# Kernel tuning notes

Hardware: AMD Instinct MI355X
Metric: run time of the kernel (lower is better)

## Reference

```python
import jax, jax.numpy as jnp
import numpy as np

N_NODES = 100000
N_EDGES = 400000
F_IN = 128
HEADS = 4
C1 = 64   # conv1 out per head
C2 = 128  # conv2 out per head
G = 2048  # num graphs
FP = 2048
HID = 64
NEG_SLOPE = 0.2


def _gat_conv(x, edge_index, W, a_src, a_dst, b, heads, ch):
    """PyG-style GATConv with self-loops, concat=True."""
    n = x.shape[0]
    loops = jnp.arange(n, dtype=edge_index.dtype)
    src = jnp.concatenate([edge_index[0], loops])
    dst = jnp.concatenate([edge_index[1], loops])
    h = (x @ W).reshape(n, heads, ch)                      # [N,H,C]
    e_src = jnp.sum(h * a_src, axis=-1)                    # [N,H]
    e_dst = jnp.sum(h * a_dst, axis=-1)                    # [N,H]
    logits = jax.nn.leaky_relu(e_src[src] + e_dst[dst], NEG_SLOPE)  # [E,H]
    m = jax.ops.segment_max(logits, dst, num_segments=n)   # per-dst max
    p = jnp.exp(logits - m[dst])
    denom = jax.ops.segment_sum(p, dst, num_segments=n)
    alpha = p / denom[dst]                                 # [E,H]
    out = jax.ops.segment_sum(h[src] * alpha[:, :, None], dst, num_segments=n)
    return out.reshape(n, heads * ch) + b


def setup_inputs() -> dict:
    key = jax.random.key(0)
    ks = jax.random.split(key, 16)
    s = 0.05
    inp = {
        "x": jax.random.normal(ks[0], (N_NODES, F_IN), jnp.float32),
        "edge_index": jax.random.randint(ks[1], (2, N_EDGES), 0, N_NODES, jnp.int32),
        "batch": jnp.sort(jax.random.randint(ks[2], (N_NODES,), 0, G, jnp.int32)),
        "fp": jax.random.normal(ks[3], (G, FP), jnp.float32),
        "W1": jax.random.normal(ks[4], (F_IN, HEADS * C1), jnp.float32) * s,
        "a_src1": jax.random.normal(ks[5], (HEADS, C1), jnp.float32) * s,
        "a_dst1": jax.random.normal(ks[6], (HEADS, C1), jnp.float32) * s,
        "b1": jnp.zeros((HEADS * C1,), jnp.float32),
        "W2": jax.random.normal(ks[7], (HEADS * C1, HEADS * C2), jnp.float32) * s,
        "a_src2": jax.random.normal(ks[8], (HEADS, C2), jnp.float32) * s,
        "a_dst2": jax.random.normal(ks[9], (HEADS, C2), jnp.float32) * s,
        "b2": jnp.zeros((HEADS * C2,), jnp.float32),
        "Wfp": jax.random.normal(ks[10], (FP, HID), jnp.float32) * s,
        "bfp": jnp.zeros((HID,), jnp.float32),
        "Wfc1": jax.random.normal(ks[11], (HEADS * C2 + HID, HID), jnp.float32) * s,
        "bfc1": jnp.zeros((HID,), jnp.float32),
        "Wfc2": jax.random.normal(ks[12], (HID, 1), jnp.float32) * s,
        "bfc2": jnp.zeros((1,), jnp.float32),
    }
    return inp


def reference(x, edge_index, batch, fp, W1, a_src1, a_dst1, b1, W2, a_src2, a_dst2, b2,
              Wfp, bfp, Wfc1, bfc1, Wfc2, bfc2):
    h = _gat_conv(x, edge_index, W1, a_src1, a_dst1, b1, HEADS, C1)
    h = jax.nn.elu(h)
    h = _gat_conv(h, edge_index, W2, a_src2, a_dst2, b2, HEADS, C2)
    h = jax.nn.elu(h)
    # global mean pool over graphs
    sums = jax.ops.segment_sum(h, batch, num_segments=G)
    counts = jax.ops.segment_sum(jnp.ones((h.shape[0], 1), h.dtype), batch, num_segments=G)
    pooled = sums / jnp.maximum(counts, 1.0)               # [G, 512]
    fph = fp @ Wfp + bfp                                   # [G, 64]
    z = jnp.concatenate([pooled, fph], axis=1)             # [G, 576]
    z = jax.nn.relu(z @ Wfc1 + bfc1)
    # dropout is identity in eval mode
    return z @ Wfc2 + bfc2                                 # [G, 1]
```

## Files before the change

### kernel.cpp

```cpp
#include <hip/hip_runtime.h>
#include <math.h>

#define NEG_SLOPE 0.2f

typedef __attribute__((ext_vector_type(8))) short bf16x8;
typedef __attribute__((ext_vector_type(4))) float f32x4;
typedef __attribute__((ext_vector_type(2))) float f32x2;

__device__ __forceinline__ float b2f(short s) {
  return __uint_as_float(((unsigned int)(unsigned short)s) << 16);
}
__device__ __forceinline__ unsigned short f2b_rne(float f) {
  unsigned int u = __float_as_uint(f);
  u = (u + 0x7FFF + ((u >> 16) & 1)) >> 16;
  return (unsigned short)u;
}

__device__ __forceinline__ void fp8x8_to_f32(uint2 raw, float* f) {
  f32x2 a = __builtin_amdgcn_cvt_pk_f32_fp8((int)raw.x, false);
  f32x2 b = __builtin_amdgcn_cvt_pk_f32_fp8((int)raw.x, true);
  f32x2 c = __builtin_amdgcn_cvt_pk_f32_fp8((int)raw.y, false);
  f32x2 d = __builtin_amdgcn_cvt_pk_f32_fp8((int)raw.y, true);
  f[0] = a[0]; f[1] = a[1]; f[2] = b[0]; f[3] = b[1];
  f[4] = c[0]; f[5] = c[1]; f[6] = d[0]; f[7] = d[1];
}

__device__ __forceinline__ void gload16(const unsigned short* g, unsigned short* l) {
  __builtin_amdgcn_global_load_lds(
      (const __attribute__((address_space(1))) unsigned int*)g,
      (__attribute__((address_space(3))) unsigned int*)l, 16, 0, 0);
}

__device__ __forceinline__ void tr_one(const float* __restrict__ W,
                                       unsigned short* __restrict__ WT,
                                       int K, int N, int idx)
{
  if (idx < K * N) {
    int k = idx / N, n = idx - k * N;
    WT[(size_t)n * K + k] = f2b_rne(W[idx]);
  }
}

__global__ __launch_bounds__(256) void prep_all(
    const float* __restrict__ x, unsigned short* __restrict__ xb, size_t nx, int B0,
    const float* __restrict__ fp, unsigned short* __restrict__ fpb, size_t nf, int B1,
    const float* __restrict__ W1, unsigned short* __restrict__ W1T,
    const float* __restrict__ W2, unsigned short* __restrict__ W2T,
    const float* __restrict__ Wfp, unsigned short* __restrict__ WfpT,
    const float* __restrict__ Wfc1, unsigned short* __restrict__ Wfc1T)
{
  int b = blockIdx.x;
  const int t = threadIdx.x;
  if (b < B0) {
    size_t i = (size_t)b * 256 + t;
    if (i < nx) xb[i] = f2b_rne(x[i]);
    return;
  }
  b -= B0;
  if (b < B1) {
    size_t i = (size_t)b * 256 + t;
    if (i < nf) fpb[i] = f2b_rne(fp[i]);
    return;
  }
  b -= B1;
  if (b < 128) { tr_one(W1, W1T, 128, 256, b * 256 + t); return; }
  b -= 128;
  if (b < 512) { tr_one(W2, W2T, 256, 512, b * 256 + t); return; }
  b -= 512;
  if (b < 512) { tr_one(Wfp, WfpT, 2048, 64, b * 256 + t); return; }
  b -= 512;
  tr_one(Wfc1, Wfc1T, 576, 64, b * 256 + t);
}

template<int EMODE>
__global__ __launch_bounds__(256) void gemm_mfma(
    const unsigned short* __restrict__ A, const unsigned short* __restrict__ BT,
    unsigned char* __restrict__ Cout, int M, int N, int K,
    const float* __restrict__ a_src, const float* __restrict__ a_dst,
    float* __restrict__ es, float* __restrict__ ed, int nh)
{
  __shared__ unsigned short As[2][128 * 32];
  __shared__ unsigned short Bs[2][128 * 32];
  const int tid  = threadIdx.x;
  const int wave = tid >> 6;
  const int lane = tid & 63;
  const int ln   = lane & 15;
  const int quad = lane >> 4;
  const int wr0  = (wave >> 1) * 64;
  const int wc0  = (wave & 1) * 64;
  const int bm   = blockIdx.y * 128;
  const int bn   = blockIdx.x * 128;

  const int sr = lane >> 2;
  const int sc = (lane & 3) * 8;
  int arow0 = bm + wave * 32 + sr;
  int arow1 = arow0 + 16;
  if (arow0 >= M) arow0 = M - 1;
  if (arow1 >= M) arow1 = M - 1;
  const unsigned short* ga0 = A + (size_t)arow0 * K + sc;
  const unsigned short* ga1 = A + (size_t)arow1 * K + sc;
  const unsigned short* gb0 = BT + (size_t)(bn + wave * 32 + sr) * K + sc;
  const unsigned short* gb1 = BT + (size_t)(bn + wave * 32 + 16 + sr) * K + sc;

  f32x4 acc[4][4];
  const f32x4 z4 = {0.f, 0.f, 0.f, 0.f};
#pragma unroll
  for (int i = 0; i < 4; ++i)
#pragma unroll
    for (int j = 0; j < 4; ++j) acc[i][j] = z4;

  {
    gload16(ga0, &As[0][wave * 1024]);
    gload16(ga1, &As[0][wave * 1024 + 512]);
    gload16(gb0, &Bs[0][wave * 1024]);
    gload16(gb1, &Bs[0][wave * 1024 + 512]);
  }

  int cur = 0;
  for (int k0 = 0; k0 < K; k0 += 32) {
    __syncthreads();
    if (k0 + 32 < K) {
      const int kn = k0 + 32;
      const int nb = cur ^ 1;
      gload16(ga0 + kn, &As[nb][wave * 1024]);
      gload16(ga1 + kn, &As[nb][wave * 1024 + 512]);
      gload16(gb0 + kn, &Bs[nb][wave * 1024]);
      gload16(gb1 + kn, &Bs[nb][wave * 1024 + 512]);
    }
    bf16x8 af[4], bfv[4];
#pragma unroll
    for (int i = 0; i < 4; ++i)
      af[i] = *(const bf16x8*)(&As[cur][(wr0 + i * 16 + ln) * 32 + quad * 8]);
#pragma unroll
    for (int j = 0; j < 4; ++j)
      bfv[j] = *(const bf16x8*)(&Bs[cur][(wc0 + j * 16 + ln) * 32 + quad * 8]);
#pragma unroll
    for (int i = 0; i < 4; ++i)
#pragma unroll
      for (int j = 0; j < 4; ++j)
        acc[i][j] = __builtin_amdgcn_mfma_f32_16x16x32_bf16(af[i], bfv[j], acc[i][j], 0, 0, 0);
    cur ^= 1;
  }
  __syncthreads();

#pragma unroll
  for (int i = 0; i < 4; ++i) {
#pragma unroll
    for (int r = 0; r < 4; ++r) {
      int row = bm + wr0 + i * 16 + quad * 4 + r;
      if (row >= M) continue;
      int p01 = __builtin_amdgcn_cvt_pk_fp8_f32(acc[i][0][r], acc[i][1][r], 0, false);
      int p23 = __builtin_amdgcn_cvt_pk_fp8_f32(acc[i][2][r], acc[i][3][r], 0, false);
      size_t rb = (size_t)row * N + bn + wc0 + ln;
      Cout[rb +  0] = (unsigned char)(p01 & 0xff);
      Cout[rb + 16] = (unsigned char)((p01 >> 8) & 0xff);
      Cout[rb + 32] = (unsigned char)(p23 & 0xff);
      Cout[rb + 48] = (unsigned char)((p23 >> 8) & 0xff);
    }
  }

  float asv[4], adv[4];
#pragma unroll
  for (int j = 0; j < 4; ++j) {
    int col = bn + wc0 + j * 16 + ln;
    asv[j] = a_src[col];
    adv[j] = a_dst[col];
  }
  if (EMODE == 64) {
    const int head = (bn + wc0) >> 6;
#pragma unroll
    for (int i = 0; i < 4; ++i) {
#pragma unroll
      for (int r = 0; r < 4; ++r) {
        float ps = 0.f, pd = 0.f;
#pragma unroll
        for (int j = 0; j < 4; ++j) {
          ps = fmaf(acc[i][j][r], asv[j], ps);
          pd = fmaf(acc[i][j][r], adv[j], pd);
        }
        for (int off = 8; off; off >>= 1) {
          ps += __shfl_down(ps, off, 16);
          pd += __shfl_down(pd, off, 16);
        }
        if (ln == 0) {
          int row = bm + wr0 + i * 16 + quad * 4 + r;
          if (row < M) {
            es[(size_t)row * nh + head] = ps;
            ed[(size_t)row * nh + head] = pd;
          }
        }
      }
    }
  } else {
    float* esp = (float*)As[0];
    float* edp = esp + 256;
#pragma unroll
    for (int i = 0; i < 4; ++i) {
#pragma unroll
      for (int r = 0; r < 4; ++r) {
        float ps = 0.f, pd = 0.f;
#pragma unroll
        for (int j = 0; j < 4; ++j) {
          ps = fmaf(acc[i][j][r], asv[j], ps);
          pd = fmaf(acc[i][j][r], adv[j], pd);
        }
        for (int off = 8; off; off >>= 1) {
          ps += __shfl_down(ps, off, 16);
          pd += __shfl_down(pd, off, 16);
        }
        if (ln == 0) {
          int rl = wr0 + i * 16 + quad * 4 + r;
          esp[rl * 2 + (wc0 >> 6)] = ps;
          edp[rl * 2 + (wc0 >> 6)] = pd;
        }
      }
    }
    __syncthreads();
    if (tid < 128) {
      int row = bm + tid;
      if (row < M) {
        int head = bn >> 7;
        es[(size_t)row * nh + head] = esp[tid * 2] + esp[tid * 2 + 1];
        ed[(size_t)row * nh + head] = edp[tid * 2] + edp[tid * 2 + 1];
      }
    }
  }
}

__global__ __launch_bounds__(256) void gemm_mfma_n64(
    const unsigned short* __restrict__ A, int lda,
    const unsigned short* __restrict__ BT, int ldb,
    float* __restrict__ Cp, int M, int kchunk)
{
  const int LDT = 72;
  __shared__ unsigned short As[128 * 72];
  __shared__ unsigned short Bs[64 * 72];
  const int tid  = threadIdx.x;
  const int wave = tid >> 6;
  const int lane = tid & 63;
  const int ln   = lane & 15;
  const int quad = lane >> 4;
  const int ks   = blockIdx.x;
  const int bm   = blockIdx.y * 128;
  const int k_beg = ks * kchunk;
  const int k_end = k_beg + kchunk;
  const int arow = tid >> 1;
  const int akb  = (tid & 1) * 32;
  const int brow = tid >> 2;
  const int bkb  = (tid & 3) * 16;

  f32x4 acc[2][4];
  const f32x4 z4 = {0.f, 0.f, 0.f, 0.f};
#pragma unroll
  for (int i = 0; i < 2; ++i)
#pragma unroll
    for (int j = 0; j < 4; ++j) acc[i][j] = z4;

  for (int k0 = k_beg; k0 < k_end; k0 += 64) {
    const unsigned short* ap = A + (size_t)(bm + arow) * lda + k0 + akb;
#pragma unroll
    for (int q = 0; q < 4; ++q)
      *(bf16x8*)(&As[arow * LDT + akb + q * 8]) = *(const bf16x8*)(ap + q * 8);
    const unsigned short* bp = BT + (size_t)brow * ldb + k0 + bkb;
#pragma unroll
    for (int q = 0; q < 2; ++q)
      *(bf16x8*)(&Bs[brow * LDT + bkb + q * 8]) = *(const bf16x8*)(bp + q * 8);
    __syncthreads();
#pragma unroll
    for (int kk = 0; kk < 2; ++kk) {
      bf16x8 af[2], bfv[4];
#pragma unroll
      for (int i = 0; i < 2; ++i)
        af[i] = *(const bf16x8*)(&As[(wave * 32 + i * 16 + ln) * LDT + kk * 32 + quad * 8]);
#pragma unroll
      for (int j = 0; j < 4; ++j)
        bfv[j] = *(const bf16x8*)(&Bs[(j * 16 + ln) * LDT + kk * 32 + quad * 8]);
#pragma unroll
      for (int i = 0; i < 2; ++i)
#pragma unroll
        for (int j = 0; j < 4; ++j)
          acc[i][j] = __builtin_amdgcn_mfma_f32_16x16x32_bf16(af[i], bfv[j], acc[i][j], 0, 0, 0);
    }
    __syncthreads();
  }
#pragma unroll
  for (int i = 0; i < 2; ++i)
#pragma unroll
    for (int r = 0; r < 4; ++r) {
      int row = bm + wave * 32 + i * 16 + quad * 4 + r;
#pragma unroll
      for (int j = 0; j < 4; ++j)
        Cp[((size_t)ks * M + row) * 64 + j * 16 + ln] = acc[i][j][r];
    }
}

__global__ void fp_finish(const float* __restrict__ Cp, int ksplit, int M,
                          const float* __restrict__ bfp,
                          unsigned short* __restrict__ zb)
{
  const int g = blockIdx.x;
  const int j = threadIdx.x;
  float s = bfp[j];
  for (int ks = 0; ks < ksplit; ++ks) s += Cp[((size_t)ks * M + g) * 64 + j];
  zb[(size_t)g * 576 + 512 + j] = f2b_rne(s);
}

__global__ void mlp_finish(const float* __restrict__ Cp, int ksplit, int M,
                           const float* __restrict__ bfc1,
                           const float* __restrict__ Wfc2, const float* __restrict__ bfc2,
                           float* __restrict__ out)
{
  const int g = blockIdx.x;
  const int j = threadIdx.x;
  float s = bfc1[j];
  for (int ks = 0; ks < ksplit; ++ks) s += Cp[((size_t)ks * M + g) * 64 + j];
  s = s > 0.f ? s : 0.f;
  float term = s * Wfc2[j];
  for (int off = 32; off; off >>= 1) term += __shfl_down(term, off, 64);
  if (j == 0) out[g] = term + bfc2[0];
}

__global__ void count_all(const int* __restrict__ ei, int E, int* __restrict__ deg,
                          const int* __restrict__ batch, int NN, int* __restrict__ gcnt,
                          int BE)
{
  int b = blockIdx.x;
  int t = threadIdx.x;
  if (b < BE) {
    int e = b * 256 + t;
    if (e < E) atomicAdd(&deg[ei[E + e]], 1);
  } else {
    int i = (b - BE) * 256 + t;
    if (i < NN) atomicAdd(&gcnt[batch[i]], 1);
  }
}

__global__ void fill_csr(const int* __restrict__ ei, int E, int* __restrict__ cursor,
                         const int* __restrict__ rowptr, int* __restrict__ csr_src)
{
  int e = blockIdx.x * 256 + threadIdx.x;
  if (e < E) {
    int d = ei[E + e];
    int pos = atomicAdd(&cursor[d], 1);
    csr_src[rowptr[d] + pos] = ei[e];
  }
}

__device__ void scan_p1_body(const int* __restrict__ vals, int n, int* __restrict__ bsum,
                             int bb)
{
  __shared__ int red[256];
  int base = bb * 1024;
  int t = threadIdx.x;
  int s = 0;
#pragma unroll
  for (int i = 0; i < 4; ++i) {
    int idx = base + i * 256 + t;
    if (idx < n) s += vals[idx];
  }
  red[t] = s;
  __syncthreads();
  for (int off = 128; off; off >>= 1) {
    if (t < off) red[t] += red[t + off];
    __syncthreads();
  }
  if (t == 0) bsum[bb] = red[0];
}

__global__ void scan2_p1(const int* __restrict__ vA, int nA, int* __restrict__ bsA, int nbA,
                         const int* __restrict__ vB, int nB, int* __restrict__ bsB)
{
  int b = blockIdx.x;
  if (b < nbA) scan_p1_body(vA, nA, bsA, b);
  else         scan_p1_body(vB, nB, bsB, b - nbA);
}

__device__ void scan_p2_body(const int* __restrict__ bsum, int* __restrict__ bpre,
                             int nb, int* __restrict__ rowptr, int n)
{
  __shared__ int tmp[128];
  int t = threadIdx.x;
  int v = (t < nb) ? bsum[t] : 0;
  tmp[t] = v;
  __syncthreads();
  for (int off = 1; off < 128; off <<= 1) {
    int add = (t >= off) ? tmp[t - off] : 0;
    __syncthreads();
    tmp[t] += add;
    __syncthreads();
  }
  if (t < nb) bpre[t] = tmp[t] - v;
  if (t == 127) rowptr[n] = tmp[127];
}

__global__ void scan2_p2(const int* __restrict__ bsA, int* __restrict__ bpA, int nbA,
                         int* __restrict__ rpA, int nA,
                         const int* __restrict__ bsB, int* __restrict__ bpB, int nbB,
                         int* __restrict__ rpB, int nB)
{
  if (blockIdx.x == 0) scan_p2_body(bsA, bpA, nbA, rpA, nA);
  else                 scan_p2_body(bsB, bpB, nbB, rpB, nB);
}

__device__ void scan_p3_body(const int* __restrict__ vals, const int* __restrict__ bpre,
                             int n, int* __restrict__ rowptr, int bb)
{
  __shared__ int tmp[256];
  int t = threadIdx.x;
  int base = bb * 1024 + t * 4;
  int v[4]; int s = 0;
#pragma unroll
  for (int i = 0; i < 4; ++i) {
    int idx = base + i;
    v[i] = (idx < n) ? vals[idx] : 0;
    s += v[i];
  }
  tmp[t] = s;
  __syncthreads();
  for (int off = 1; off < 256; off <<= 1) {
    int add = (t >= off) ? tmp[t - off] : 0;
    __syncthreads();
    tmp[t] += add;
    __syncthreads();
  }
  int run = bpre[bb] + tmp[t] - s;
#pragma unroll
  for (int i = 0; i < 4; ++i) {
    int idx = base + i;
    if (idx < n) rowptr[idx] = run;
    run += v[i];
  }
}

__global__ void scan2_p3(const int* __restrict__ vA, const int* __restrict__ bpA, int nA,
                         int* __restrict__ rpA, int nbA,
                         const int* __restrict__ vB, const int* __restrict__ bpB, int nB,
                         int* __restrict__ rpB)
{
  int b = blockIdx.x;
  if (b < nbA) scan_p3_body(vA, bpA, nA, rpA, b);
  else         scan_p3_body(vB, bpB, nB, rpB, b - nbA);
}

__global__ void alpha_kernel(const float* __restrict__ es, const float* __restrict__ ed,
                             const int* __restrict__ rowptr, const int* __restrict__ csr_src,
                             float* __restrict__ w_csr, float* __restrict__ wself,
                             float* __restrict__ dinv, int N, int nh)
{
  int idx = blockIdx.x * 256 + threadIdx.x;
  if (idx >= N * nh) return;
  const int dst = idx / nh;
  const int h = idx - dst * nh;
  const float edh = ed[(size_t)dst * nh + h];
  const int beg = rowptr[dst], end = rowptr[dst + 1];
  float sum = 0.f;
  for (int e = beg; e < end; ++e) {
    int s = csr_src[e];
    float l = es[(size_t)s * nh + h] + edh;
    l = l >= 0.f ? l : NEG_SLOPE * l;
    float w = expf(l);
    w_csr[(size_t)e * nh + h] = w;
    sum += w;
  }
  float ls = es[(size_t)dst * nh + h] + edh;
  ls = ls >= 0.f ? ls : NEG_SLOPE * ls;
  float wsl = expf(ls);
  sum += wsl;
  wself[(size_t)dst * nh + h] = wsl;
  dinv[(size_t)dst * nh + h] = 1.0f / sum;
}

__global__ __launch_bounds__(256) void aggregate_b(
    const unsigned char* __restrict__ h,
    const float* __restrict__ w_csr, const float* __restrict__ wself,
    const float* __restrict__ dinv,
    const int* __restrict__ rowptr, const int* __restrict__ csr_src,
    const float* __restrict__ bias, unsigned short* __restrict__ out,
    int N, int nh, int C)
{
  const int HC = nh * C;
  const int CH8 = HC >> 3;
  const int dpb = 256 / CH8;
  const int grp = threadIdx.x / CH8;
  const int lane = threadIdx.x - grp * CH8;
  const int dst = blockIdx.x * dpb + grp;
  if (dst >= N) return;
  const int ch = lane << 3;
  const int head = ch / C;
  const int beg = rowptr[dst], end = rowptr[dst + 1];
  float acc[8] = {0.f, 0.f, 0.f, 0.f, 0.f, 0.f, 0.f, 0.f};
  float hv[8];
  int e = beg;
  for (; e + 1 < end; e += 2) {
    int s0 = csr_src[e], s1 = csr_src[e + 1];
    float a0 = w_csr[(size_t)e * nh + head];
    float a1 = w_csr[(size_t)(e + 1) * nh + head];
    uint2 r0 = *(const uint2*)(h + (size_t)s0 * HC + ch);
    uint2 r1 = *(const uint2*)(h + (size_t)s1 * HC + ch);
    fp8x8_to_f32(r0, hv);
#pragma unroll
    for (int r = 0; r < 8; ++r) acc[r] = fmaf(a0, hv[r], acc[r]);
    fp8x8_to_f32(r1, hv);
#pragma unroll
    for (int r = 0; r < 8; ++r) acc[r] = fmaf(a1, hv[r], acc[r]);
  }
  if (e < end) {
    int s0 = csr_src[e];
    float a0 = w_csr[(size_t)e * nh + head];
    uint2 r0 = *(const uint2*)(h + (size_t)s0 * HC + ch);
    fp8x8_to_f32(r0, hv);
#pragma unroll
    for (int r = 0; r < 8; ++r) acc[r] = fmaf(a0, hv[r], acc[r]);
  }
  {
    float a = wself[(size_t)dst * nh + head];
    uint2 r0 = *(const uint2*)(h + (size_t)dst * HC + ch);
    fp8x8_to_f32(r0, hv);
#pragma unroll
    for (int r = 0; r < 8; ++r) acc[r] = fmaf(a, hv[r], acc[r]);
  }
  const float di = dinv[(size_t)dst * nh + head];
  bf16x8 o;
#pragma unroll
  for (int r = 0; r < 8; ++r) {
    float v = acc[r] * di + bias[ch + r];
    v = v > 0.f ? v : (expf(v) - 1.0f);
    o[r] = (short)f2b_rne(v);
  }
  *(bf16x8*)(out + (size_t)dst * HC + ch) = o;
}

__global__ __launch_bounds__(256) void agg_pool(
    const unsigned char* __restrict__ h,
    const float* __restrict__ w_csr, const float* __restrict__ wself,
    const float* __restrict__ dinv,
    const int* __restrict__ rowptr, const int* __restrict__ csr_src,
    const float* __restrict__ bias, const int* __restrict__ grp,
    unsigned short* __restrict__ zb)
{
  const int g = blockIdx.x;
  const int wave = threadIdx.x >> 6;
  const int lane = threadIdx.x & 63;
  const int ch = lane << 3;
  const int head = lane >> 4;
  const int gbeg = grp[g], gend = grp[g + 1];
  float bch[8];
#pragma unroll
  for (int r = 0; r < 8; ++r) bch[r] = bias[ch + r];
  float pool[8] = {0.f, 0.f, 0.f, 0.f, 0.f, 0.f, 0.f, 0.f};
  float hv[8];

  for (int node = gbeg + wave; node < gend; node += 4) {
    const int beg = rowptr[node], end = rowptr[node + 1];
    float acc[8] = {0.f, 0.f, 0.f, 0.f, 0.f, 0.f, 0.f, 0.f};
    int e = beg;
    for (; e + 1 < end; e += 2) {
      int s0 = csr_src[e], s1 = csr_src[e + 1];
      float a0 = w_csr[(size_t)e * 4 + head];
      float a1 = w_csr[(size_t)(e + 1) * 4 + head];
      uint2 r0 = *(const uint2*)(h + (size_t)s0 * 512 + ch);
      uint2 r1 = *(const uint2*)(h + (size_t)s1 * 512 + ch);
      fp8x8_to_f32(r0, hv);
#pragma unroll
      for (int r = 0; r < 8; ++r) acc[r] = fmaf(a0, hv[r], acc[r]);
      fp8x8_to_f32(r1, hv);
#pragma unroll
      for (int r = 0; r < 8; ++r) acc[r] = fmaf(a1, hv[r], acc[r]);
    }
    if (e < end) {
      int s0 = csr_src[e];
      float a0 = w_csr[(size_t)e * 4 + head];
      uint2 r0 = *(const uint2*)(h + (size_t)s0 * 512 + ch);
      fp8x8_to_f32(r0, hv);
#pragma unroll
      for (int r = 0; r < 8; ++r) acc[r] = fmaf(a0, hv[r], acc[r]);
    }
    {
      float a = wself[(size_t)node * 4 + head];
      uint2 r0 = *(const uint2*)(h + (size_t)node * 512 + ch);
      fp8x8_to_f32(r0, hv);
#pragma unroll
      for (int r = 0; r < 8; ++r) acc[r] = fmaf(a, hv[r], acc[r]);
    }
    const float di = dinv[(size_t)node * 4 + head];
#pragma unroll
    for (int r = 0; r < 8; ++r) {
      float v = acc[r] * di + bch[r];
      v = v > 0.f ? v : (expf(v) - 1.0f);
      pool[r] += v;
    }
  }

  __shared__ float red[4][512];
#pragma unroll
  for (int r = 0; r < 8; ++r) red[wave][ch + r] = pool[r];
  __syncthreads();
  const float inv = 1.0f / (float)max(gend - gbeg, 1);
#pragma unroll
  for (int k = 0; k < 2; ++k) {
    int c = threadIdx.x + k * 256;
    float s = (red[0][c] + red[1][c]) + (red[2][c] + red[3][c]);
    zb[(size_t)g * 576 + c] = f2b_rne(s * inv);
  }
}

extern "C" void kernel_launch(void* const* d_in, const int* in_sizes, int n_in,
                              void* d_out, int out_size, void* d_ws, size_t ws_size,
                              hipStream_t stream)
{
  const float* x      = (const float*)d_in[0];
  const int*   ei     = (const int*)d_in[1];
  const int*   batch  = (const int*)d_in[2];
  const float* fp     = (const float*)d_in[3];
  const float* W1     = (const float*)d_in[4];
  const float* a_src1 = (const float*)d_in[5];
  const float* a_dst1 = (const float*)d_in[6];
  const float* b1     = (const float*)d_in[7];
  const float* W2     = (const float*)d_in[8];
  const float* a_src2 = (const float*)d_in[9];
  const float* a_dst2 = (const float*)d_in[10];
  const float* b2     = (const float*)d_in[11];
  const float* Wfp    = (const float*)d_in[12];
  const float* bfp    = (const float*)d_in[13];
  const float* Wfc1   = (const float*)d_in[14];
  const float* bfc1   = (const float*)d_in[15];
  const float* Wfc2   = (const float*)d_in[16];
  const float* bfc2   = (const float*)d_in[17];
  float* out = (float*)d_out;

  const int NN = in_sizes[0] / 128;
  const int E  = in_sizes[1] / 2;
  const int G  = in_sizes[3] / 2048;
  const int FIN = 128, H = 4, C1 = 64, C2 = 128;
  const int HC1 = H * C1;
  const int HC2 = H * C2;
  const int KFP = in_sizes[3] / G;
  const int KZ  = HC2 + 64;
  const int KS_FP = 16;
  const int KS_Z  = 9;

  char* base = (char*)d_ws;
  size_t off = 0;
  auto alloc = [&](size_t bytes) {
    char* p = base + off; off += (bytes + 255) & ~(size_t)255; return p;
  };
  size_t xb_sz  = ((size_t)NN * FIN * 2 + 255) & ~(size_t)255;
  size_t h1b_sz = (size_t)NN * HC1;
  size_t h2b_sz = (size_t)NN * HC2;
  size_t rA = xb_sz + h1b_sz; if (h2b_sz > rA) rA = h2b_sz;
  char* RA = alloc(rA);
  unsigned short* xb  = (unsigned short*)RA;
  unsigned char*  h1b = (unsigned char*)(RA + xb_sz);
  unsigned char*  h2b = (unsigned char*)RA;
  size_t fpb_sz  = ((size_t)G * KFP * 2 + 255) & ~(size_t)255;
  size_t cpfp_sz = (size_t)KS_FP * G * 64 * 4;
  size_t agg1_sz = (size_t)NN * HC1 * 2;
  size_t rB = fpb_sz + cpfp_sz; if (agg1_sz > rB) rB = agg1_sz;
  char* RB = alloc(rB);
  unsigned short* fpb   = (unsigned short*)RB;
  float*          Cp_fp = (float*)(RB + fpb_sz);
  unsigned short* agg1b = (unsigned short*)RB;
  float* w1     = (float*)alloc((size_t)E * H * 4);
  float* wself1 = (float*)alloc((size_t)NN * H * 4);
  float* es1    = (float*)alloc((size_t)NN * H * 4);
  float* ed1    = (float*)alloc((size_t)NN * H * 4);
  float* dinv1  = (float*)alloc((size_t)NN * H * 4);
  float* w2 = w1, *wself2 = wself1, *es2 = es1, *ed2 = ed1, *dinv2 = dinv1;
  unsigned short* zb    = (unsigned short*)alloc((size_t)G * KZ * 2);
  float*          Cp_z  = (float*)alloc((size_t)KS_Z * G * 64 * 4);
  unsigned short* W1T   = (unsigned short*)alloc((size_t)HC1 * FIN * 2);
  unsigned short* W2T   = (unsigned short*)alloc((size_t)HC2 * HC1 * 2);
  unsigned short* WfpT  = (unsigned short*)alloc((size_t)64 * KFP * 2);
  unsigned short* Wfc1T = (unsigned short*)alloc((size_t)64 * KZ * 2);
  int* iarena   = (int*)alloc(((size_t)2 * NN + G) * 4);
  int* deg      = iarena;
  int* cursor   = iarena + NN;
  int* gcnt     = iarena + 2 * NN;
  int* rowptr_n = (int*)alloc(((size_t)NN + 1) * 4);
  int* rowptr_g = (int*)alloc(((size_t)G + 1) * 4);
  int* csr_src  = (int*)alloc((size_t)E * 4);
  int* bsumA    = (int*)alloc(128 * 4);
  int* bpreA    = (int*)alloc(128 * 4);
  int* bsumB    = (int*)alloc(128 * 4);
  int* bpreB    = (int*)alloc(128 * 4);

  const size_t nx = (size_t)NN * FIN;
  const size_t nf = (size_t)G * KFP;
  const int B0 = (int)((nx + 255) / 256);
  const int B1 = (int)((nf + 255) / 256);
  {
    int nb = B0 + B1 + 128 + 512 + 512 + 144;
    prep_all<<<nb, 256, 0, stream>>>(x, xb, nx, B0, fp, fpb, nf, B1,
                                     W1, W1T, W2, W2T, Wfp, WfpT, Wfc1, Wfc1T);
  }

  {
    dim3 gg(KS_FP, G / 128);
    gemm_mfma_n64<<<gg, 256, 0, stream>>>(fpb, KFP, WfpT, KFP, Cp_fp, G, KFP / KS_FP);
    fp_finish<<<G, 64, 0, stream>>>(Cp_fp, KS_FP, G, bfp, zb);
  }

  hipMemsetAsync(iarena, 0, sizeof(int) * ((size_t)2 * NN + G), stream);
  {
    int BE = (E + 255) / 256;
    int BN = (NN + 255) / 256;
    count_all<<<BE + BN, 256, 0, stream>>>(ei, E, deg, batch, NN, gcnt, BE);
  }
  {
    int nbA = (NN + 1023) / 1024;
    int nbB = (G + 1023) / 1024;
    scan2_p1<<<nbA + nbB, 256, 0, stream>>>(deg, NN, bsumA, nbA, gcnt, G, bsumB);
    scan2_p2<<<2, 128, 0, stream>>>(bsumA, bpreA, nbA, rowptr_n, NN,
                                    bsumB, bpreB, nbB, rowptr_g, G);
    scan2_p3<<<nbA + nbB, 256, 0, stream>>>(deg, bpreA, NN, rowptr_n, nbA,
                                            gcnt, bpreB, G, rowptr_g);
  }
  fill_csr<<<(E + 255) / 256, 256, 0, stream>>>(ei, E, cursor, rowptr_n, csr_src);

  {
    dim3 gg(HC1 / 128, (NN + 127) / 128);
    gemm_mfma<64><<<gg, 256, 0, stream>>>(xb, W1T, h1b, NN, HC1, FIN,
                                          a_src1, a_dst1, es1, ed1, H);
  }
  alpha_kernel<<<(NN * H + 255) / 256, 256, 0, stream>>>(es1, ed1, rowptr_n, csr_src,
                                                         w1, wself1, dinv1, NN, H);
  aggregate_b<<<(NN + 7) / 8, 256, 0, stream>>>(h1b, w1, wself1, dinv1, rowptr_n, csr_src,
                                                b1, agg1b, NN, H, C1);

  {
    dim3 gg(HC2 / 128, (NN + 127) / 128);
    gemm_mfma<128><<<gg, 256, 0, stream>>>(agg1b, W2T, h2b, NN, HC2, HC1,
                                           a_src2, a_dst2, es2, ed2, H);
  }
  alpha_kernel<<<(NN * H + 255) / 256, 256, 0, stream>>>(es2, ed2, rowptr_n, csr_src,
                                                         w2, wself2, dinv2, NN, H);
  agg_pool<<<G, 256, 0, stream>>>(h2b, w2, wself2, dinv2, rowptr_n, csr_src,
                                  b2, rowptr_g, zb);

  {
    dim3 gg(KS_Z, G / 128);
    gemm_mfma_n64<<<gg, 256, 0, stream>>>(zb, KZ, Wfc1T, KZ, Cp_z, G, KZ / KS_Z);
    mlp_finish<<<G, 64, 0, stream>>>(Cp_z, KS_Z, G, bfc1, Wfc2, bfc2, out);
  }
}
```

Measured before the change: 459.6 us.

## Deepen GEMM pipeline to four stages with swizzled LDS and XCD-aware block mapping

```diff
diff --git a/kernel.cpp b/kernel.cpp
--- a/kernel.cpp
+++ b/kernel.cpp
@@ -29,6 +29,10 @@
   __builtin_amdgcn_global_load_lds(
       (const __attribute__((address_space(1))) unsigned int*)g,
       (__attribute__((address_space(3))) unsigned int*)l, 16, 0, 0);
+}
+
+template<int N> __device__ __forceinline__ void vmwait() {
+  asm volatile("s_waitcnt vmcnt(%0)" :: "n"(N) : "memory");
 }
 
 __device__ __forceinline__ void tr_one(const float* __restrict__ W,
@@ -72,15 +76,16 @@
   tr_one(Wfc1, Wfc1T, 576, 64, b * 256 + t);
 }
 
-template<int EMODE>
+template<int EMODE, int KK>
 __global__ __launch_bounds__(256) void gemm_mfma(
     const unsigned short* __restrict__ A, const unsigned short* __restrict__ BT,
-    unsigned char* __restrict__ Cout, int M, int N, int K,
+    unsigned char* __restrict__ Cout, int M, int N,
     const float* __restrict__ a_src, const float* __restrict__ a_dst,
     float* __restrict__ es, float* __restrict__ ed, int nh)
 {
-  __shared__ unsigned short As[2][128 * 32];
-  __shared__ unsigned short Bs[2][128 * 32];
+  constexpr int NT = KK / 32;
+  __shared__ unsigned short As[4][128 * 32];
+  __shared__ unsigned short Bs[4][128 * 32];
   const int tid  = threadIdx.x;
   const int wave = tid >> 6;
   const int lane = tid & 63;
@@ -88,19 +93,35 @@
   const int quad = lane >> 4;
   const int wr0  = (wave >> 1) * 64;
   const int wc0  = (wave & 1) * 64;
-  const int bm   = blockIdx.y * 128;
-  const int bn   = blockIdx.x * 128;
-
-  const int sr = lane >> 2;
-  const int sc = (lane & 3) * 8;
-  int arow0 = bm + wave * 32 + sr;
-  int arow1 = arow0 + 16;
-  if (arow0 >= M) arow0 = M - 1;
-  if (arow1 >= M) arow1 = M - 1;
-  const unsigned short* ga0 = A + (size_t)arow0 * K + sc;
-  const unsigned short* ga1 = A + (size_t)arow1 * K + sc;
-  const unsigned short* gb0 = BT + (size_t)(bn + wave * 32 + sr) * K + sc;
-  const unsigned short* gb1 = BT + (size_t)(bn + wave * 32 + 16 + sr) * K + sc;
+
+  const int nwg = gridDim.x;
+  const int ncol = N >> 7;
+  const int bid = blockIdx.x;
+  const int qq = nwg >> 3, rr = nwg & 7;
+  const int xc = bid & 7, io = bid >> 3;
+  const int swz = (xc < rr ? xc * (qq + 1) : rr * (qq + 1) + (xc - rr) * qq) + io;
+  const int bn = (swz % ncol) * 128;
+  const int bm = (swz / ncol) * 128;
+
+  const int srow = lane >> 2;
+  const int cch  = lane & 3;
+  const int rt0  = wave * 32 + srow;
+  const int ksw  = ((cch ^ (srow & 3)) << 3);
+  int ar0 = bm + rt0;      if (ar0 >= M) ar0 = M - 1;
+  int ar1 = bm + rt0 + 16; if (ar1 >= M) ar1 = M - 1;
+  const unsigned short* gA0 = A + (size_t)ar0 * KK + ksw;
+  const unsigned short* gA1 = A + (size_t)ar1 * KK + ksw;
+  const unsigned short* gB0 = BT + (size_t)(bn + rt0) * KK + ksw;
+  const unsigned short* gB1 = BT + (size_t)(bn + rt0 + 16) * KK + ksw;
+
+  auto stage = [&](int T) {
+    const int b = T & 3;
+    const int kk = T * 32;
+    gload16(gA0 + kk, &As[b][(wave * 32) * 32]);
+    gload16(gA1 + kk, &As[b][(wave * 32 + 16) * 32]);
+    gload16(gB0 + kk, &Bs[b][(wave * 32) * 32]);
+    gload16(gB1 + kk, &Bs[b][(wave * 32 + 16) * 32]);
+  };
 
   f32x4 acc[4][4];
   const f32x4 z4 = {0.f, 0.f, 0.f, 0.f};
@@ -109,39 +130,37 @@
 #pragma unroll
     for (int j = 0; j < 4; ++j) acc[i][j] = z4;
 
-  {
-    gload16(ga0, &As[0][wave * 1024]);
-    gload16(ga1, &As[0][wave * 1024 + 512]);
-    gload16(gb0, &Bs[0][wave * 1024]);
-    gload16(gb1, &Bs[0][wave * 1024 + 512]);
-  }
-
-  int cur = 0;
-  for (int k0 = 0; k0 < K; k0 += 32) {
-    __syncthreads();
-    if (k0 + 32 < K) {
-      const int kn = k0 + 32;
-      const int nb = cur ^ 1;
-      gload16(ga0 + kn, &As[nb][wave * 1024]);
-      gload16(ga1 + kn, &As[nb][wave * 1024 + 512]);
-      gload16(gb0 + kn, &Bs[nb][wave * 1024]);
-      gload16(gb1 + kn, &Bs[nb][wave * 1024 + 512]);
-    }
+  stage(0); stage(1); stage(2);
+
+#pragma unroll
+  for (int t = 0; t < NT; ++t) {
+    if (t + 3 < NT) stage(t + 3);
+    if      (t < NT - 3) vmwait<12>();
+    else if (t == NT - 3) vmwait<8>();
+    else if (t == NT - 2) vmwait<4>();
+    else                  vmwait<0>();
+    __builtin_amdgcn_s_barrier();
+    __builtin_amdgcn_sched_barrier(0);
+    const int b = t & 3;
     bf16x8 af[4], bfv[4];
 #pragma unroll
-    for (int i = 0; i < 4; ++i)
-      af[i] = *(const bf16x8*)(&As[cur][(wr0 + i * 16 + ln) * 32 + quad * 8]);
-#pragma unroll
-    for (int j = 0; j < 4; ++j)
-      bfv[j] = *(const bf16x8*)(&Bs[cur][(wc0 + j * 16 + ln) * 32 + quad * 8]);
+    for (int i = 0; i < 4; ++i) {
+      const int row = wr0 + i * 16 + ln;
+      af[i] = *(const bf16x8*)(&As[b][row * 32 + ((quad ^ (ln & 3)) << 3)]);
+    }
+#pragma unroll
+    for (int j = 0; j < 4; ++j) {
+      const int row = wc0 + j * 16 + ln;
+      bfv[j] = *(const bf16x8*)(&Bs[b][row * 32 + ((quad ^ (ln & 3)) << 3)]);
+    }
 #pragma unroll
     for (int i = 0; i < 4; ++i)
 #pragma unroll
       for (int j = 0; j < 4; ++j)
         acc[i][j] = __builtin_amdgcn_mfma_f32_16x16x32_bf16(af[i], bfv[j], acc[i][j], 0, 0, 0);
-    cur ^= 1;
-  }
-  __syncthreads();
+    __builtin_amdgcn_sched_barrier(0);
+    __builtin_amdgcn_s_barrier();
+  }
 
 #pragma unroll
   for (int i = 0; i < 4; ++i) {
@@ -718,9 +737,9 @@
   fill_csr<<<(E + 255) / 256, 256, 0, stream>>>(ei, E, cursor, rowptr_n, csr_src);
 
   {
-    dim3 gg(HC1 / 128, (NN + 127) / 128);
-    gemm_mfma<64><<<gg, 256, 0, stream>>>(xb, W1T, h1b, NN, HC1, FIN,
-                                          a_src1, a_dst1, es1, ed1, H);
+    const int nrow = (NN + 127) / 128;
+    gemm_mfma<64, 128><<<nrow * (HC1 / 128), 256, 0, stream>>>(
+        xb, W1T, h1b, NN, HC1, a_src1, a_dst1, es1, ed1, H);
   }
   alpha_kernel<<<(NN * H + 255) / 256, 256, 0, stream>>>(es1, ed1, rowptr_n, csr_src,
                                                          w1, wself1, dinv1, NN, H);
@@ -728,9 +747,9 @@
                                                 b1, agg1b, NN, H, C1);
 
   {
-    dim3 gg(HC2 / 128, (NN + 127) / 128);
-    gemm_mfma<128><<<gg, 256, 0, stream>>>(agg1b, W2T, h2b, NN, HC2, HC1,
-                                           a_src2, a_dst2, es2, ed2, H);
+    const int nrow = (NN + 127) / 128;
+    gemm_mfma<128, 256><<<nrow * (HC2 / 128), 256, 0, stream>>>(
+        agg1b, W2T, h2b, NN, HC2, a_src2, a_dst2, es2, ed2, H);
   }
   alpha_kernel<<<(NN * H + 255) / 256, 256, 0, stream>>>(es2, ed2, rowptr_n, csr_src,
                                                          w2, wself2, dinv2, NN, H);
```

Measured after the change: 461.6 us. About the same (+0.4%).
